# Optimization experiments

Measured on AMD Instinct MI355X. Metric: run time of the kernel, lower is better.

## Reference

```python
import jax, jax.numpy as jnp
import numpy as np

BSZ, T, ENC, HID = 128, 512, 128, 128


def setup_inputs() -> dict:
    key = jax.random.key(0)
    ks = jax.random.split(key, 8)
    encoder_output = jax.random.normal(ks[0], (BSZ, T, ENC), dtype=jnp.float32)
    lengths = jax.random.randint(ks[1], (BSZ,), 4, T + 1)
    mask = (jnp.arange(T)[None, :] < lengths[:, None]).astype(jnp.int32)
    s = 1.0 / np.sqrt(HID)  # torch LSTM init range
    W_ih = jax.random.uniform(ks[2], (4 * HID, ENC), jnp.float32, -s, s)
    W_hh = jax.random.uniform(ks[3], (4 * HID, HID), jnp.float32, -s, s)
    b_ih = jax.random.uniform(ks[4], (4 * HID,), jnp.float32, -s, s)
    b_hh = jax.random.uniform(ks[5], (4 * HID,), jnp.float32, -s, s)
    s2 = 1.0 / np.sqrt(HID + ENC)  # torch Linear init range
    fc_w = jax.random.uniform(ks[6], (1, HID + ENC), jnp.float32, -s2, s2)
    fc_b = jax.random.uniform(ks[7], (1,), jnp.float32, -s2, s2)
    return {"encoder_output": encoder_output, "mask": mask, "W_ih": W_ih,
            "W_hh": W_hh, "b_ih": b_ih, "b_hh": b_hh, "fc_w": fc_w, "fc_b": fc_b}


def _lstm_last(src, W_ih, W_hh, b_ih, b_hh):
    # src: [N, 3, E] -> last hidden state [N, H]; torch gate order i,f,g,o
    N = src.shape[0]
    H = W_hh.shape[1]
    h0 = jnp.zeros((N, H), src.dtype)
    c0 = jnp.zeros((N, H), src.dtype)

    def step(carry, x):
        h, c = carry
        gates = x @ W_ih.T + h @ W_hh.T + b_ih + b_hh
        i, f, g, o = jnp.split(gates, 4, axis=-1)
        c = jax.nn.sigmoid(f) * c + jax.nn.sigmoid(i) * jnp.tanh(g)
        h = jax.nn.sigmoid(o) * jnp.tanh(c)
        return (h, c), None

    (h, _), _ = jax.lax.scan(step, (h0, c0), jnp.swapaxes(src, 0, 1))
    return h


def reference(encoder_output, mask, W_ih, W_hh, b_ih, b_hh, fc_w, fc_b):
    B, Tn, E = encoder_output.shape
    H = W_hh.shape[1]
    lengths = jnp.sum(mask, axis=1)                       # [B]
    J = Tn - 3                                            # number of window starts
    # his_turn_states: encoder_output zeroed beyond each length
    states = encoder_output * mask[..., None].astype(encoder_output.dtype)
    # sliding windows of 3 consecutive turn states: [B, J, 3, E]
    src = jnp.stack([states[:, 0:J], states[:, 1:J + 1], states[:, 2:J + 2]], axis=2)
    h_last = _lstm_last(src.reshape(B * J, 3, E), W_ih, W_hh, b_ih, b_hh)
    h_last = h_last.reshape(B, J, H)                      # [B, J, H]
    # con_fc(concat(h, tgt)) decomposes: w_h.h + w_e.tgt + b
    w = fc_w[0]
    a = h_last @ w[:H]                                    # [B, J]
    cterm = states @ w[H:]                                # [B, T]
    logits = a[:, :, None] + cterm[:, None, :] + fc_b[0]  # [B, J, T]
    j_idx = jnp.arange(J)
    k_idx = jnp.arange(Tn)
    valid_k = (k_idx[None, None, :] >= (j_idx[None, :, None] + 3)) & \
              (k_idx[None, None, :] < lengths[:, None, None])    # candidate mask
    valid_pair = (j_idx[None, :] <= (lengths[:, None] - 4))       # [B, J]
    neg = jnp.asarray(-1e9, logits.dtype)
    lse = jax.nn.logsumexp(jnp.where(valid_k, logits, neg), axis=-1)  # [B, J]
    pos_idx = jnp.broadcast_to((j_idx + 3)[None, :, None], (B, J, 1))
    pos = jnp.take_along_axis(logits, pos_idx, axis=2)[..., 0]        # [B, J]
    loss_pair = lse - pos                                 # CE with target index 0
    vp = valid_pair.astype(logits.dtype)
    dli_loss = jnp.sum(loss_pair * vp) / jnp.sum(vp)
    return dli_loss
```

## Files before the change

kernel.cpp:

```cpp
#include <hip/hip_runtime.h>
#include <math.h>

#define BSZ 128
#define T   512
#define E   128
#define H   128
#define TPB 512

__global__ __launch_bounds__(TPB) void dli_row_kernel(
    const float* __restrict__ enc,
    const int*   __restrict__ mask,
    const float* __restrict__ fc_w,
    double*      __restrict__ accum)
{
    const int b    = blockIdx.x;
    const int t    = threadIdx.x;
    const int lane = t & 63;
    const int wid  = t >> 6;

    __shared__ float s_c[T];
    __shared__ float s_e[T];
    __shared__ float s_red[8];
    __shared__ int   s_len;

    if (t == 0) s_len = 0;
    __syncthreads();

    int mv = mask[b * T + t];
    unsigned long long bal = __ballot(mv != 0);
    if (lane == 0) atomicAdd(&s_len, __popcll(bal));

    const float we0 = fc_w[H + 2 * lane];
    const float we1 = fc_w[H + 2 * lane + 1];
    const float* rowp = enc + (size_t)b * T * E;
    for (int k = wid; k < T; k += 8) {
        float2 v = *reinterpret_cast<const float2*>(rowp + k * E + 2 * lane);
        float p = v.x * we0 + v.y * we1;
        #pragma unroll
        for (int off = 32; off >= 1; off >>= 1)
            p += __shfl_xor(p, off);
        if (lane == 0) s_c[k] = p;
    }
    __syncthreads();
    const int len = s_len;

    float mval = (t >= 3 && t < len) ? s_c[t] : -INFINITY;
    #pragma unroll
    for (int off = 32; off >= 1; off >>= 1)
        mval = fmaxf(mval, __shfl_xor(mval, off));
    if (lane == 0) s_red[wid] = mval;
    __syncthreads();
    if (t == 0) {
        float m = s_red[0];
        #pragma unroll
        for (int i = 1; i < 8; i++) m = fmaxf(m, s_red[i]);
        s_red[0] = m;
    }
    __syncthreads();
    const float Mrow = s_red[0];

    s_e[t] = (t >= 3 && t < len) ? expf(s_c[t] - Mrow) : 0.0f;
    __syncthreads();

    for (int d = 1; d < T; d <<= 1) {
        float add = (t + d < T) ? s_e[t + d] : 0.0f;
        __syncthreads();
        s_e[t] += add;
        __syncthreads();
    }

    float term = 0.0f;
    if (t >= 3 && t < len)
        term = Mrow + logf(s_e[t]) - s_c[t];
    #pragma unroll
    for (int off = 32; off >= 1; off >>= 1)
        term += __shfl_xor(term, off);
    if (lane == 0) s_red[wid] = term;
    __syncthreads();
    if (t == 0) {
        float rs = 0.0f;
        #pragma unroll
        for (int i = 0; i < 8; i++) rs += s_red[i];
        int cnt = len - 3; if (cnt < 0) cnt = 0;
        atomicAdd(&accum[0], (double)rs);
        atomicAdd(&accum[1], (double)cnt);
    }
}

__global__ void dli_final(const double* __restrict__ accum,
                          float* __restrict__ out)
{
    out[0] = (float)(accum[0] / accum[1]);
}

extern "C" void kernel_launch(void* const* d_in, const int* in_sizes, int n_in,
                              void* d_out, int out_size, void* d_ws, size_t ws_size,
                              hipStream_t stream) {
    const float* enc  = (const float*)d_in[0];
    const int*   mask = (const int*)d_in[1];
    const float* fc_w = (const float*)d_in[6];

    double* accum = (double*)d_ws;
    hipMemsetAsync(d_ws, 0, 2 * sizeof(double), stream);

    dli_row_kernel<<<BSZ, TPB, 0, stream>>>(enc, mask, fc_w, accum);
    dli_final<<<1, 1, 0, stream>>>(accum, (float*)d_out);
}
```

Measured before the change: 113.9 us.

## Split dot-product into separate wide-grid kernel, skip masked rows

```diff
diff --git a/kernel.cpp b/kernel.cpp
--- a/kernel.cpp
+++ b/kernel.cpp
@@ -5,12 +5,34 @@
 #define T   512
 #define E   128
 #define H   128
-#define TPB 512
 
-__global__ __launch_bounds__(TPB) void dli_row_kernel(
+__global__ __launch_bounds__(256) void dli_dot_kernel(
     const float* __restrict__ enc,
     const int*   __restrict__ mask,
     const float* __restrict__ fc_w,
+    float*       __restrict__ cterm)
+{
+    const int t    = threadIdx.x;
+    const int lane = t & 63;
+    const int wid  = t >> 6;
+    const int sub  = lane >> 5;
+    const int li   = lane & 31;
+    const long row = (long)blockIdx.x * 8 + wid * 2 + sub;
+
+    if (mask[row] == 0) return;
+
+    const float4 w4 = *reinterpret_cast<const float4*>(fc_w + H + 4 * li);
+    const float4 v  = *reinterpret_cast<const float4*>(enc + row * E + 4 * li);
+    float p = v.x * w4.x + v.y * w4.y + v.z * w4.z + v.w * w4.w;
+    #pragma unroll
+    for (int off = 16; off >= 1; off >>= 1)
+        p += __shfl_xor(p, off);
+    if (li == 0) cterm[row] = p;
+}
+
+__global__ __launch_bounds__(T) void dli_scan_kernel(
+    const float* __restrict__ cterm,
+    const int*   __restrict__ mask,
     double*      __restrict__ accum)
 {
     const int b    = blockIdx.x;
@@ -26,21 +48,11 @@
     if (t == 0) s_len = 0;
     __syncthreads();
 
-    int mv = mask[b * T + t];
+    const int mv = mask[b * T + t];
     unsigned long long bal = __ballot(mv != 0);
     if (lane == 0) atomicAdd(&s_len, __popcll(bal));
 
-    const float we0 = fc_w[H + 2 * lane];
-    const float we1 = fc_w[H + 2 * lane + 1];
-    const float* rowp = enc + (size_t)b * T * E;
-    for (int k = wid; k < T; k += 8) {
-        float2 v = *reinterpret_cast<const float2*>(rowp + k * E + 2 * lane);
-        float p = v.x * we0 + v.y * we1;
-        #pragma unroll
-        for (int off = 32; off >= 1; off >>= 1)
-            p += __shfl_xor(p, off);
-        if (lane == 0) s_c[k] = p;
-    }
+    s_c[t] = mv ? cterm[b * T + t] : 0.0f;
     __syncthreads();
     const int len = s_len;
 
@@ -101,8 +113,10 @@
     const float* fc_w = (const float*)d_in[6];
 
     double* accum = (double*)d_ws;
+    float*  cterm = (float*)((char*)d_ws + 16);
     hipMemsetAsync(d_ws, 0, 2 * sizeof(double), stream);
 
-    dli_row_kernel<<<BSZ, TPB, 0, stream>>>(enc, mask, fc_w, accum);
+    dli_dot_kernel<<<(BSZ * T) / 8, 256, 0, stream>>>(enc, mask, fc_w, cterm);
+    dli_scan_kernel<<<BSZ, T, 0, stream>>>(cterm, mask, accum);
     dli_final<<<1, 1, 0, stream>>>(accum, (float*)d_out);
 }
```

Measured after the change: 95.99 us. -15.7%, faster.
